# Optimization experiments

Hardware: AMD Instinct MI355X
Metric: run time of the kernel (lower is better)

Reference implementation:

```python
import jax, jax.numpy as jnp
import numpy as np

N_NODES = 50000
N_EDGES = 800000
GNN_IN, GNN_HID, GNN_OUT = 64, 128, 64
MLP_HID, MLP_OUT = 128, 1
EDGE_DIST_DIM = 16
NEG_SLOPE = 0.2


def setup_inputs() -> dict:
    key = jax.random.key(0)
    ks = jax.random.split(key, 16)
    inp = {
        "x": jax.random.normal(ks[0], (N_NODES, GNN_IN), dtype=jnp.float32),
        "edge_index": jax.random.randint(ks[1], (N_EDGES, 2), 0, N_NODES, dtype=jnp.int32),
        "edge_dist": jax.random.normal(ks[2], (N_EDGES, EDGE_DIST_DIM), dtype=jnp.float32),
        # GATConv layer 1
        "W_g1": jax.random.normal(ks[3], (GNN_IN, GNN_HID), dtype=jnp.float32) / np.sqrt(GNN_IN),
        "a1_src": jax.random.normal(ks[4], (GNN_HID,), dtype=jnp.float32) / np.sqrt(GNN_HID),
        "a1_dst": jax.random.normal(ks[5], (GNN_HID,), dtype=jnp.float32) / np.sqrt(GNN_HID),
        "b_g1": jnp.zeros((GNN_HID,), dtype=jnp.float32),
        # GATConv layer 2
        "W_g2": jax.random.normal(ks[6], (GNN_HID, GNN_OUT), dtype=jnp.float32) / np.sqrt(GNN_HID),
        "a2_src": jax.random.normal(ks[7], (GNN_OUT,), dtype=jnp.float32) / np.sqrt(GNN_OUT),
        "a2_dst": jax.random.normal(ks[8], (GNN_OUT,), dtype=jnp.float32) / np.sqrt(GNN_OUT),
        "b_g2": jnp.zeros((GNN_OUT,), dtype=jnp.float32),
        # edge MLP: in = (GNN_IN + GNN_OUT)*2 + EDGE_DIST_DIM = 272
        "W_m1": jax.random.normal(ks[9], ((GNN_IN + GNN_OUT) * 2 + EDGE_DIST_DIM, MLP_HID), dtype=jnp.float32) / np.sqrt((GNN_IN + GNN_OUT) * 2 + EDGE_DIST_DIM),
        "b_m1": jnp.zeros((MLP_HID,), dtype=jnp.float32),
        "W_m2": jax.random.normal(ks[10], (MLP_HID, MLP_OUT), dtype=jnp.float32) / np.sqrt(MLP_HID),
        "b_m2": jnp.zeros((MLP_OUT,), dtype=jnp.float32),
    }
    return inp


def gat_conv(x, src, dst, W, a_src, a_dst, bias, n_nodes):
    """Single-head GATConv (PyG defaults: self-loops already included in src/dst)."""
    h = x @ W                                # (N, out)
    alpha_s = h @ a_src                      # (N,)
    alpha_d = h @ a_dst                      # (N,)
    e = jax.nn.leaky_relu(alpha_s[src] + alpha_d[dst], NEG_SLOPE)  # (E,)
    # segment softmax over incoming edges of each destination node
    e_max = jax.ops.segment_max(e, dst, num_segments=n_nodes)
    w = jnp.exp(e - e_max[dst])
    denom = jax.ops.segment_sum(w, dst, num_segments=n_nodes)
    alpha = w / (denom[dst] + 1e-16)
    out = jax.ops.segment_sum(alpha[:, None] * h[src], dst, num_segments=n_nodes)
    return out + bias


def reference(x, edge_index, edge_dist,
              W_g1, a1_src, a1_dst, b_g1,
              W_g2, a2_src, a2_dst, b_g2,
              W_m1, b_m1, W_m2, b_m2):
    n = x.shape[0]
    row = edge_index[:, 0]
    col = edge_index[:, 1]
    # undirected edges + self loops (PyG GATConv add_self_loops=True)
    loops = jnp.arange(n, dtype=edge_index.dtype)
    src = jnp.concatenate([row, col, loops])
    dst = jnp.concatenate([col, row, loops])

    f = jax.nn.relu(gat_conv(x, src, dst, W_g1, a1_src, a1_dst, b_g1, n))
    f = jax.nn.relu(gat_conv(f, src, dst, W_g2, a2_src, a2_dst, b_g2, n))

    xf = jnp.concatenate([x, f], axis=1)     # (N, gnn_in+gnn_out)
    edge_attr = jnp.concatenate([xf[row], xf[col], edge_dist], axis=1)  # (E, 272)
    h = jax.nn.relu(edge_attr @ W_m1 + b_m1)
    return jax.nn.sigmoid(h @ W_m2 + b_m2)   # (E, 1)
```

## Files before the change

kernel.cpp:

```cpp
#include <hip/hip_runtime.h>
#include <hip/hip_bf16.h>
#include <math.h>


#define GIN 64
#define GHID 128
#define GOUT 64

typedef unsigned int u32;
typedef unsigned short u16;

__device__ __forceinline__ float bflo(u32 u) {
  union { u32 i; float f; } c; c.i = u << 16; return c.f;
}
__device__ __forceinline__ float bfhi(u32 u) {
  union { u32 i; float f; } c; c.i = u & 0xffff0000u; return c.f;
}
__device__ __forceinline__ u16 f2bf(float x) {
  __hip_bfloat16 h = __float2bfloat16(x);
  return *reinterpret_cast<u16*>(&h);
}


__global__ void hist_kernel(const int* __restrict__ eidx, int* __restrict__ deg,
                            int nE, int n) {
  int tot = 2 * nE + n;
  for (int i = blockIdx.x * blockDim.x + threadIdx.x; i < tot;
       i += gridDim.x * blockDim.x) {
    int dst;
    if (i < nE) dst = eidx[2 * i + 1];
    else if (i < 2 * nE) dst = eidx[2 * (i - nE)];
    else dst = i - 2 * nE;
    atomicAdd(&deg[dst], 1);
  }
}

#define SCAN_CHUNK 1024
__global__ void scan_partial(const int* __restrict__ deg, int* __restrict__ bsum,
                             int n) {
  int b = blockIdx.x, tid = threadIdx.x;
  int base = b * SCAN_CHUNK + tid * 4;
  int s = 0;
#pragma unroll
  for (int c = 0; c < 4; ++c) { int i = base + c; if (i < n) s += deg[i]; }
#pragma unroll
  for (int off = 32; off; off >>= 1) s += __shfl_xor(s, off, 64);
  __shared__ int ws[4];
  if ((tid & 63) == 0) ws[tid >> 6] = s;
  __syncthreads();
  if (tid == 0) bsum[b] = ws[0] + ws[1] + ws[2] + ws[3];
}
__global__ void scan_bsums(const int* __restrict__ bsum, int* __restrict__ bscan,
                           int* __restrict__ offs, int nb, int n) {
  int lane = threadIdx.x;
  int v = (lane < nb) ? bsum[lane] : 0;
  int incl = v;
#pragma unroll
  for (int off = 1; off < 64; off <<= 1) {
    int t = __shfl_up(incl, off, 64);
    if (lane >= off) incl += t;
  }
  if (lane < nb) bscan[lane] = incl - v;
  if (lane == 63) offs[n] = incl;
}
__global__ void scan_final(const int* __restrict__ deg, const int* __restrict__ bscan,
                           int* __restrict__ offs, int* __restrict__ cursor, int n) {
  int b = blockIdx.x, tid = threadIdx.x;
  int base = b * SCAN_CHUNK + tid * 4;
  int v[4]; int s = 0;
#pragma unroll
  for (int c = 0; c < 4; ++c) { int i = base + c; v[c] = (i < n) ? deg[i] : 0; s += v[c]; }
  int lane = tid & 63, wv = tid >> 6;
  int incl = s;
#pragma unroll
  for (int off = 1; off < 64; off <<= 1) {
    int t = __shfl_up(incl, off, 64);
    if (lane >= off) incl += t;
  }
  __shared__ int ws[4];
  if (lane == 63) ws[wv] = incl;
  __syncthreads();
  int woff = 0;
  for (int w2 = 0; w2 < wv; ++w2) woff += ws[w2];
  int excl = bscan[b] + woff + incl - s;
#pragma unroll
  for (int c = 0; c < 4; ++c) {
    int i = base + c;
    if (i < n) { offs[i] = excl; cursor[i] = excl; }
    excl += v[c];
  }
}

__global__ void scatter_kernel(const int* __restrict__ eidx, int* __restrict__ cursor,
                               int* __restrict__ csr, int nE, int n) {
  int tot = 2 * nE + n;
  for (int i = blockIdx.x * blockDim.x + threadIdx.x; i < tot;
       i += gridDim.x * blockDim.x) {
    int src, dst;
    if (i < nE)          { src = eidx[2 * i];            dst = eidx[2 * i + 1]; }
    else if (i < 2 * nE) { src = eidx[2 * (i - nE) + 1]; dst = eidx[2 * (i - nE)]; }
    else                 { src = i - 2 * nE;             dst = src; }
    int pos = atomicAdd(&cursor[dst], 1);
    csr[pos] = src;
  }
}


template <bool SCORES>
__global__ __launch_bounds__(256) void gemm_bf(
    const float* __restrict__ A, const float* __restrict__ A2, int ksp,
    int lda, int lda2,
    const float* __restrict__ B, int bskip, int ldb,
    u16* __restrict__ Cb, int ldcb,
    const float* __restrict__ av, const float* __restrict__ bv,
    float* __restrict__ as_, float* __restrict__ ad_,
    int M, int K) {
  __shared__ float As[32][68];
  __shared__ float Bs[32][64];
  int tid = threadIdx.x;
  int m0 = blockIdx.x * 64;
  int n0 = blockIdx.y * 64;
  const float* Bp = B + (size_t)(n0 >> 7) * bskip;
  int nb0 = n0 & 127;
  int tx = tid & 15, ty = tid >> 4;
  float acc[4][4] = {};
  for (int k0 = 0; k0 < K; k0 += 32) {
    const float* Asrc; int Alda; int kk;
    if (k0 < ksp) { Asrc = A;  Alda = lda;  kk = k0; }
    else          { Asrc = A2; Alda = lda2; kk = k0 - ksp; }
#pragma unroll
    for (int r = 0; r < 2; ++r) {
      int m = (tid >> 3) + r * 32;
      int k = (tid & 7) * 4;
      float4 v = make_float4(0.f, 0.f, 0.f, 0.f);
      int gm = m0 + m;
      if (gm < M) v = *reinterpret_cast<const float4*>(&Asrc[(size_t)gm * Alda + kk + k]);
      As[k + 0][m] = v.x; As[k + 1][m] = v.y; As[k + 2][m] = v.z; As[k + 3][m] = v.w;
    }
#pragma unroll
    for (int r = 0; r < 2; ++r) {
      int k = (tid >> 4) + r * 16;
      int nn = (tid & 15) * 4;
      float4 v = *reinterpret_cast<const float4*>(&Bp[(size_t)(k0 + k) * ldb + nb0 + nn]);
      *reinterpret_cast<float4*>(&Bs[k][nn]) = v;
    }
    __syncthreads();
#pragma unroll
    for (int k = 0; k < 32; ++k) {
      float a[4], b[4];
#pragma unroll
      for (int i = 0; i < 4; ++i) a[i] = As[k][ty * 4 + i];
#pragma unroll
      for (int i = 0; i < 4; ++i) b[i] = Bs[k][tx * 4 + i];
#pragma unroll
      for (int i = 0; i < 4; ++i)
#pragma unroll
        for (int j = 0; j < 4; ++j) acc[i][j] += a[i] * b[j];
    }
    __syncthreads();
  }
  float avv[4], bvv[4];
  if constexpr (SCORES) {
#pragma unroll
    for (int j = 0; j < 4; ++j) {
      avv[j] = av[n0 + tx * 4 + j];
      bvv[j] = bv[n0 + tx * 4 + j];
    }
  }
#pragma unroll
  for (int i = 0; i < 4; ++i) {
    int gm = m0 + ty * 4 + i;
    bool inb = gm < M;
    if (inb) {
      u16* bp = &Cb[(size_t)gm * ldcb + n0 + tx * 4];
      *reinterpret_cast<ushort4*>(bp) = make_ushort4(
          f2bf(acc[i][0]), f2bf(acc[i][1]), f2bf(acc[i][2]), f2bf(acc[i][3]));
    }
    if constexpr (SCORES) {
      float ps = acc[i][0] * avv[0] + acc[i][1] * avv[1] +
                 acc[i][2] * avv[2] + acc[i][3] * avv[3];
      float pd = acc[i][0] * bvv[0] + acc[i][1] * bvv[1] +
                 acc[i][2] * bvv[2] + acc[i][3] * bvv[3];
#pragma unroll
      for (int off = 1; off < 16; off <<= 1) {
        ps += __shfl_xor(ps, off, 16);
        pd += __shfl_xor(pd, off, 16);
      }
      if (tx == 0 && inb) {
        atomicAdd(&as_[gm], ps);
        atomicAdd(&ad_[gm], pd);
      }
    }
  }
}


__global__ __launch_bounds__(256) void gat_agg1(
    const u16* __restrict__ hb, const float* __restrict__ as_,
    const float* __restrict__ ad_, const int* __restrict__ offs,
    const int* __restrict__ csr, const float* __restrict__ bias,
    float* __restrict__ out, int n) {
  int node = blockIdx.x * 4 + (threadIdx.x >> 6);
  if (node >= n) return;
  int lane = threadIdx.x & 63;
  int g = lane >> 5, sl = lane & 31;
  int beg = offs[node], end = offs[node + 1];
  float adn = ad_[node];
  float m = -1e30f;
  for (int i = beg + lane; i < end; i += 64) {
    float v = as_[csr[i]] + adn;
    v = (v > 0.f) ? v : 0.2f * v;
    m = fmaxf(m, v);
  }
#pragma unroll
  for (int off = 32; off; off >>= 1) m = fmaxf(m, __shfl_xor(m, off, 64));
  float denom = 0.f;
  float a[4] = {0.f, 0.f, 0.f, 0.f};
  int i = beg + g;
  int s = (i < end) ? csr[i] : -1;
  uint2 pv = make_uint2(0, 0); float e = 0.f;
  if (s >= 0) {
    pv = *reinterpret_cast<const uint2*>(&hb[(size_t)s * 128 + sl * 4]);
    e = as_[s] + adn;
  }
  while (s >= 0) {
    int i2 = i + 2;
    int s2 = (i2 < end) ? csr[i2] : -1;
    uint2 pv2 = make_uint2(0, 0); float e2 = 0.f;
    if (s2 >= 0) {
      pv2 = *reinterpret_cast<const uint2*>(&hb[(size_t)s2 * 128 + sl * 4]);
      e2 = as_[s2] + adn;
    }
    e = (e > 0.f) ? e : 0.2f * e;
    float wgt = __expf(e - m);
    denom += wgt;
    a[0] += wgt * bflo(pv.x); a[1] += wgt * bfhi(pv.x);
    a[2] += wgt * bflo(pv.y); a[3] += wgt * bfhi(pv.y);
    i = i2; s = s2; pv = pv2; e = e2;
  }
  denom += __shfl_xor(denom, 32, 64);
#pragma unroll
  for (int j = 0; j < 4; ++j) a[j] += __shfl_xor(a[j], 32, 64);
  if (g == 0) {
    float inv = 1.f / (denom + 1e-16f);
    float4 bv4 = *reinterpret_cast<const float4*>(&bias[sl * 4]);
    float4 o;
    o.x = fmaxf(a[0] * inv + bv4.x, 0.f);
    o.y = fmaxf(a[1] * inv + bv4.y, 0.f);
    o.z = fmaxf(a[2] * inv + bv4.z, 0.f);
    o.w = fmaxf(a[3] * inv + bv4.w, 0.f);
    *reinterpret_cast<float4*>(&out[(size_t)node * 128 + sl * 4]) = o;
  }
}


__global__ __launch_bounds__(256) void gat_agg2(
    const u16* __restrict__ hb, const float* __restrict__ as_,
    const float* __restrict__ ad_, const int* __restrict__ offs,
    const int* __restrict__ csr, const float* __restrict__ bias,
    float* __restrict__ out, int n) {
  int node = blockIdx.x * 4 + (threadIdx.x >> 6);
  if (node >= n) return;
  int lane = threadIdx.x & 63;
  int g = lane >> 4, sl = lane & 15;
  int beg = offs[node], end = offs[node + 1];
  float adn = ad_[node];
  float m = -1e30f;
  for (int i = beg + lane; i < end; i += 64) {
    float v = as_[csr[i]] + adn;
    v = (v > 0.f) ? v : 0.2f * v;
    m = fmaxf(m, v);
  }
#pragma unroll
  for (int off = 32; off; off >>= 1) m = fmaxf(m, __shfl_xor(m, off, 64));
  float denom = 0.f;
  float a[4] = {0.f, 0.f, 0.f, 0.f};
  int i = beg + g;
  int s = (i < end) ? csr[i] : -1;
  uint2 pv = make_uint2(0, 0); float e = 0.f;
  if (s >= 0) {
    pv = *reinterpret_cast<const uint2*>(&hb[(size_t)s * 64 + sl * 4]);
    e = as_[s] + adn;
  }
  while (s >= 0) {
    int i2 = i + 4;
    int s2 = (i2 < end) ? csr[i2] : -1;
    uint2 pv2 = make_uint2(0, 0); float e2 = 0.f;
    if (s2 >= 0) {
      pv2 = *reinterpret_cast<const uint2*>(&hb[(size_t)s2 * 64 + sl * 4]);
      e2 = as_[s2] + adn;
    }
    e = (e > 0.f) ? e : 0.2f * e;
    float wgt = __expf(e - m);
    denom += wgt;
    a[0] += wgt * bflo(pv.x); a[1] += wgt * bfhi(pv.x);
    a[2] += wgt * bflo(pv.y); a[3] += wgt * bfhi(pv.y);
    i = i2; s = s2; pv = pv2; e = e2;
  }
  denom += __shfl_xor(denom, 16, 64);
  denom += __shfl_xor(denom, 32, 64);
#pragma unroll
  for (int j = 0; j < 4; ++j) {
    a[j] += __shfl_xor(a[j], 16, 64);
    a[j] += __shfl_xor(a[j], 32, 64);
  }
  if (lane < 16) {
    float inv = 1.f / (denom + 1e-16f);
    float4 bv4 = *reinterpret_cast<const float4*>(&bias[sl * 4]);
    float4 o;
    o.x = fmaxf(a[0] * inv + bv4.x, 0.f);
    o.y = fmaxf(a[1] * inv + bv4.y, 0.f);
    o.z = fmaxf(a[2] * inv + bv4.z, 0.f);
    o.w = fmaxf(a[3] * inv + bv4.w, 0.f);
    *reinterpret_cast<float4*>(&out[(size_t)node * 64 + sl * 4]) = o;
  }
}


__global__ __launch_bounds__(256) void edge_mlp(
    const int* __restrict__ eidx, const float* __restrict__ dist,
    const u16* __restrict__ Pb, const float* __restrict__ W3,
    const float* __restrict__ b1, const float* __restrict__ W2,
    const float* __restrict__ b2, float* __restrict__ out, int nE) {
  __shared__ float4 W3s[16][32];
  int tid = threadIdx.x;
  for (int idx = tid; idx < 16 * 32; idx += 256) {
    int k = idx >> 5, q = idx & 31;
    W3s[k][q] = *reinterpret_cast<const float4*>(&W3[k * 128 + q * 4]);
  }
  __syncthreads();
  int lane = tid & 63, wv = tid >> 6;
  int g = lane >> 4, sl = lane & 15;
  float4 b1a = *reinterpret_cast<const float4*>(&b1[sl * 8]);
  float4 b1b = *reinterpret_cast<const float4*>(&b1[sl * 8 + 4]);
  float4 w2a = *reinterpret_cast<const float4*>(&W2[sl * 8]);
  float4 w2b = *reinterpret_cast<const float4*>(&W2[sl * 8 + 4]);
  float b2v = b2[0];
  for (int e0 = (blockIdx.x * 4 + wv) * 4; e0 < nE; e0 += gridDim.x * 16) {
    int e = e0 + g;
    bool valid = e < nE;
    int ee = valid ? e : 0;
    int r = eidx[2 * ee], c = eidx[2 * ee + 1];
    uint4 p1 = *reinterpret_cast<const uint4*>(&Pb[(size_t)r * 256 + sl * 8]);
    uint4 p2 = *reinterpret_cast<const uint4*>(&Pb[(size_t)c * 256 + 128 + sl * 8]);
    float dsl = dist[(size_t)ee * 16 + sl];
    float a[8];
    a[0] = bflo(p1.x) + bflo(p2.x) + b1a.x;
    a[1] = bfhi(p1.x) + bfhi(p2.x) + b1a.y;
    a[2] = bflo(p1.y) + bflo(p2.y) + b1a.z;
    a[3] = bfhi(p1.y) + bfhi(p2.y) + b1a.w;
    a[4] = bflo(p1.z) + bflo(p2.z) + b1b.x;
    a[5] = bfhi(p1.z) + bfhi(p2.z) + b1b.y;
    a[6] = bflo(p1.w) + bflo(p2.w) + b1b.z;
    a[7] = bfhi(p1.w) + bfhi(p2.w) + b1b.w;
#pragma unroll
    for (int k = 0; k < 16; ++k) {
      float dk = __shfl(dsl, (g << 4) + k, 64);
      float4 wA = W3s[k][2 * sl];
      float4 wB = W3s[k][2 * sl + 1];
      a[0] += dk * wA.x; a[1] += dk * wA.y; a[2] += dk * wA.z; a[3] += dk * wA.w;
      a[4] += dk * wB.x; a[5] += dk * wB.y; a[6] += dk * wB.z; a[7] += dk * wB.w;
    }
    float p = fmaxf(a[0], 0.f) * w2a.x + fmaxf(a[1], 0.f) * w2a.y +
              fmaxf(a[2], 0.f) * w2a.z + fmaxf(a[3], 0.f) * w2a.w +
              fmaxf(a[4], 0.f) * w2b.x + fmaxf(a[5], 0.f) * w2b.y +
              fmaxf(a[6], 0.f) * w2b.z + fmaxf(a[7], 0.f) * w2b.w;
#pragma unroll
    for (int off = 1; off < 16; off <<= 1) p += __shfl_xor(p, off, 16);
    if (valid && sl == 0) out[e] = 1.f / (1.f + __expf(-(p + b2v)));
  }
}


extern "C" void kernel_launch(void* const* d_in, const int* in_sizes, int n_in,
                              void* d_out, int out_size, void* d_ws, size_t ws_size,
                              hipStream_t stream) {
  const float* x      = (const float*)d_in[0];
  const int*   eidx   = (const int*)d_in[1];
  const float* dist   = (const float*)d_in[2];
  const float* W_g1   = (const float*)d_in[3];
  const float* a1_src = (const float*)d_in[4];
  const float* a1_dst = (const float*)d_in[5];
  const float* b_g1   = (const float*)d_in[6];
  const float* W_g2   = (const float*)d_in[7];
  const float* a2_src = (const float*)d_in[8];
  const float* a2_dst = (const float*)d_in[9];
  const float* b_g2   = (const float*)d_in[10];
  const float* W_m1   = (const float*)d_in[11];
  const float* b_m1   = (const float*)d_in[12];
  const float* W_m2   = (const float*)d_in[13];
  const float* b_m2   = (const float*)d_in[14];
  float* out = (float*)d_out;

  const int n  = in_sizes[0] / GIN;
  const int nE = in_sizes[1] / 2;
  const int ndir = 2 * nE + n;

  char* w = (char*)d_ws;
  size_t off = 0;
  auto alloc = [&](size_t bytes) {
    size_t o = off;
    off += (bytes + 255) & ~(size_t)255;
    return o;
  };
  size_t o_deg    = alloc((size_t)n * 4);
  size_t o_offs   = alloc((size_t)(n + 1) * 4);
  size_t o_cursor = alloc((size_t)n * 4);
  size_t o_as1    = alloc((size_t)n * 4);
  size_t o_ad1    = alloc((size_t)n * 4);
  size_t o_as2    = alloc((size_t)n * 4);
  size_t o_ad2    = alloc((size_t)n * 4);
  size_t o_bsum   = alloc(64 * 4);
  size_t o_bscan  = alloc(64 * 4);
  size_t o_csr    = alloc((size_t)ndir * 4);
  size_t o_big    = alloc((size_t)n * 256 * 2);
  size_t o_f1     = alloc((size_t)n * GHID * 4);
  size_t o_f2     = alloc((size_t)n * GOUT * 4);
  (void)ws_size;

  int*   deg    = (int*)(w + o_deg);
  int*   offs   = (int*)(w + o_offs);
  int*   cursor = (int*)(w + o_cursor);
  float* as1    = (float*)(w + o_as1);
  float* ad1    = (float*)(w + o_ad1);
  float* as2    = (float*)(w + o_as2);
  float* ad2    = (float*)(w + o_ad2);
  int*   bsum   = (int*)(w + o_bsum);
  int*   bscan  = (int*)(w + o_bscan);
  int*   csr    = (int*)(w + o_csr);
  u16*   h1b    = (u16*)(w + o_big);
  u16*   h2b    = (u16*)(w + o_big + (size_t)n * GHID * 2);
  u16*   Pb     = (u16*)(w + o_big);
  float* f1     = (float*)(w + o_f1);
  float* f2     = (float*)(w + o_f2);

  hipMemsetAsync(deg, 0, (size_t)n * 4, stream);
  hipMemsetAsync(as1, 0, (size_t)n * 4, stream);
  hipMemsetAsync(ad1, 0, (size_t)n * 4, stream);
  hipMemsetAsync(as2, 0, (size_t)n * 4, stream);
  hipMemsetAsync(ad2, 0, (size_t)n * 4, stream);
  hist_kernel<<<2048, 256, 0, stream>>>(eidx, deg, nE, n);
  int nb = (n + SCAN_CHUNK - 1) / SCAN_CHUNK;
  scan_partial<<<nb, 256, 0, stream>>>(deg, bsum, n);
  scan_bsums<<<1, 64, 0, stream>>>(bsum, bscan, offs, nb, n);
  scan_final<<<nb, 256, 0, stream>>>(deg, bscan, offs, cursor, n);
  scatter_kernel<<<2048, 256, 0, stream>>>(eidx, cursor, csr, nE, n);

  const int mtiles = (n + 63) / 64;
  const int BIGK = 1 << 30;

  gemm_bf<true><<<dim3(mtiles, 2), 256, 0, stream>>>(
      x, x, BIGK, GIN, GIN, W_g1, 0, GHID, h1b, GHID,
      a1_src, a1_dst, as1, ad1, n, GIN);

  gat_agg1<<<(n + 3) / 4, 256, 0, stream>>>(h1b, as1, ad1, offs, csr, b_g1, f1, n);

  gemm_bf<true><<<dim3(mtiles, 1), 256, 0, stream>>>(
      f1, f1, BIGK, GHID, GHID, W_g2, 0, GOUT, h2b, GOUT,
      a2_src, a2_dst, as2, ad2, n, GHID);

  gat_agg2<<<(n + 3) / 4, 256, 0, stream>>>(h2b, as2, ad2, offs, csr, b_g2, f2, n);

  gemm_bf<false><<<dim3(mtiles, 4), 256, 0, stream>>>(
      x, f2, GIN, GIN, GOUT, W_m1, 128 * 128, GHID, Pb, 256,
      nullptr, nullptr, nullptr, nullptr, n, GHID);

  edge_mlp<<<4096, 256, 0, stream>>>(eidx, dist, Pb, W_m1 + 256 * 128, b_m1, W_m2, b_m2,
                                     out, nE);
}
```

Measured before the change: 719.1 us.

## Sort edges by source for MLP locality, widen GAT gathers, drop softmax max pass

Adds a counting sort of the original edges by source row (a histogram, scan and scatter into ra/ce arrays), so the edge MLP visits edges grouped by source node and reuses the Pb row loads. The GAT aggregation kernels now load 16-byte bf16 vectors per lane and process more edges per wave in parallel. They also drop the max-subtraction pass of the segment softmax, which risks exp overflow for large logits. The sort adds several kernels and extra workspace, and the edge_mlp reads of dist and writes of out become scattered.

```diff
diff --git a/kernel.cpp b/kernel.cpp
--- a/kernel.cpp
+++ b/kernel.cpp
@@ -32,6 +32,14 @@
     else if (i < 2 * nE) dst = eidx[2 * (i - nE)];
     else dst = i - 2 * nE;
     atomicAdd(&deg[dst], 1);
+  }
+}
+
+__global__ void hist_r(const int* __restrict__ eidx, int* __restrict__ deg2,
+                       int nE) {
+  for (int e = blockIdx.x * blockDim.x + threadIdx.x; e < nE;
+       e += gridDim.x * blockDim.x) {
+    atomicAdd(&deg2[eidx[2 * e]], 1);
   }
 }
 
@@ -102,6 +110,17 @@
     else                 { src = i - 2 * nE;             dst = src; }
     int pos = atomicAdd(&cursor[dst], 1);
     csr[pos] = src;
+  }
+}
+
+__global__ void scatter_r(const int* __restrict__ eidx, int* __restrict__ cur2,
+                          int* __restrict__ ra, int2* __restrict__ ce, int nE) {
+  for (int e = blockIdx.x * blockDim.x + threadIdx.x; e < nE;
+       e += gridDim.x * blockDim.x) {
+    int r = eidx[2 * e], c = eidx[2 * e + 1];
+    int pos = atomicAdd(&cur2[r], 1);
+    ra[pos] = r;
+    ce[pos] = make_int2(c, e);
   }
 }
 
@@ -203,53 +222,57 @@
   int node = blockIdx.x * 4 + (threadIdx.x >> 6);
   if (node >= n) return;
   int lane = threadIdx.x & 63;
-  int g = lane >> 5, sl = lane & 31;
+  int g = lane >> 4, sl = lane & 15;
   int beg = offs[node], end = offs[node + 1];
   float adn = ad_[node];
-  float m = -1e30f;
-  for (int i = beg + lane; i < end; i += 64) {
-    float v = as_[csr[i]] + adn;
-    v = (v > 0.f) ? v : 0.2f * v;
-    m = fmaxf(m, v);
-  }
-#pragma unroll
-  for (int off = 32; off; off >>= 1) m = fmaxf(m, __shfl_xor(m, off, 64));
   float denom = 0.f;
-  float a[4] = {0.f, 0.f, 0.f, 0.f};
+  float a[8] = {};
   int i = beg + g;
   int s = (i < end) ? csr[i] : -1;
-  uint2 pv = make_uint2(0, 0); float e = 0.f;
+  uint4 pv = make_uint4(0, 0, 0, 0); float e = 0.f;
   if (s >= 0) {
-    pv = *reinterpret_cast<const uint2*>(&hb[(size_t)s * 128 + sl * 4]);
+    pv = *reinterpret_cast<const uint4*>(&hb[(size_t)s * 128 + sl * 8]);
     e = as_[s] + adn;
   }
   while (s >= 0) {
-    int i2 = i + 2;
+    int i2 = i + 4;
     int s2 = (i2 < end) ? csr[i2] : -1;
-    uint2 pv2 = make_uint2(0, 0); float e2 = 0.f;
+    uint4 pv2 = make_uint4(0, 0, 0, 0); float e2 = 0.f;
     if (s2 >= 0) {
-      pv2 = *reinterpret_cast<const uint2*>(&hb[(size_t)s2 * 128 + sl * 4]);
+      pv2 = *reinterpret_cast<const uint4*>(&hb[(size_t)s2 * 128 + sl * 8]);
       e2 = as_[s2] + adn;
     }
     e = (e > 0.f) ? e : 0.2f * e;
-    float wgt = __expf(e - m);
+    float wgt = __expf(e);
     denom += wgt;
     a[0] += wgt * bflo(pv.x); a[1] += wgt * bfhi(pv.x);
     a[2] += wgt * bflo(pv.y); a[3] += wgt * bfhi(pv.y);
+    a[4] += wgt * bflo(pv.z); a[5] += wgt * bfhi(pv.z);
+    a[6] += wgt * bflo(pv.w); a[7] += wgt * bfhi(pv.w);
     i = i2; s = s2; pv = pv2; e = e2;
   }
+  denom += __shfl_xor(denom, 16, 64);
   denom += __shfl_xor(denom, 32, 64);
 #pragma unroll
-  for (int j = 0; j < 4; ++j) a[j] += __shfl_xor(a[j], 32, 64);
+  for (int j = 0; j < 8; ++j) {
+    a[j] += __shfl_xor(a[j], 16, 64);
+    a[j] += __shfl_xor(a[j], 32, 64);
+  }
   if (g == 0) {
     float inv = 1.f / (denom + 1e-16f);
-    float4 bv4 = *reinterpret_cast<const float4*>(&bias[sl * 4]);
-    float4 o;
-    o.x = fmaxf(a[0] * inv + bv4.x, 0.f);
-    o.y = fmaxf(a[1] * inv + bv4.y, 0.f);
-    o.z = fmaxf(a[2] * inv + bv4.z, 0.f);
-    o.w = fmaxf(a[3] * inv + bv4.w, 0.f);
-    *reinterpret_cast<float4*>(&out[(size_t)node * 128 + sl * 4]) = o;
+    float4 b0 = *reinterpret_cast<const float4*>(&bias[sl * 8]);
+    float4 b1v = *reinterpret_cast<const float4*>(&bias[sl * 8 + 4]);
+    float4 o0, o1;
+    o0.x = fmaxf(a[0] * inv + b0.x, 0.f);
+    o0.y = fmaxf(a[1] * inv + b0.y, 0.f);
+    o0.z = fmaxf(a[2] * inv + b0.z, 0.f);
+    o0.w = fmaxf(a[3] * inv + b0.w, 0.f);
+    o1.x = fmaxf(a[4] * inv + b1v.x, 0.f);
+    o1.y = fmaxf(a[5] * inv + b1v.y, 0.f);
+    o1.z = fmaxf(a[6] * inv + b1v.z, 0.f);
+    o1.w = fmaxf(a[7] * inv + b1v.w, 0.f);
+    *reinterpret_cast<float4*>(&out[(size_t)node * 128 + sl * 8]) = o0;
+    *reinterpret_cast<float4*>(&out[(size_t)node * 128 + sl * 8 + 4]) = o1;
   }
 }
 
@@ -262,63 +285,66 @@
   int node = blockIdx.x * 4 + (threadIdx.x >> 6);
   if (node >= n) return;
   int lane = threadIdx.x & 63;
-  int g = lane >> 4, sl = lane & 15;
+  int g = lane >> 3, sl = lane & 7;
   int beg = offs[node], end = offs[node + 1];
   float adn = ad_[node];
-  float m = -1e30f;
-  for (int i = beg + lane; i < end; i += 64) {
-    float v = as_[csr[i]] + adn;
-    v = (v > 0.f) ? v : 0.2f * v;
-    m = fmaxf(m, v);
-  }
-#pragma unroll
-  for (int off = 32; off; off >>= 1) m = fmaxf(m, __shfl_xor(m, off, 64));
   float denom = 0.f;
-  float a[4] = {0.f, 0.f, 0.f, 0.f};
+  float a[8] = {};
   int i = beg + g;
   int s = (i < end) ? csr[i] : -1;
-  uint2 pv = make_uint2(0, 0); float e = 0.f;
+  uint4 pv = make_uint4(0, 0, 0, 0); float e = 0.f;
   if (s >= 0) {
-    pv = *reinterpret_cast<const uint2*>(&hb[(size_t)s * 64 + sl * 4]);
+    pv = *reinterpret_cast<const uint4*>(&hb[(size_t)s * 64 + sl * 8]);
     e = as_[s] + adn;
   }
   while (s >= 0) {
-    int i2 = i + 4;
+    int i2 = i + 8;
     int s2 = (i2 < end) ? csr[i2] : -1;
-    uint2 pv2 = make_uint2(0, 0); float e2 = 0.f;
+    uint4 pv2 = make_uint4(0, 0, 0, 0); float e2 = 0.f;
     if (s2 >= 0) {
-      pv2 = *reinterpret_cast<const uint2*>(&hb[(size_t)s2 * 64 + sl * 4]);
+      pv2 = *reinterpret_cast<const uint4*>(&hb[(size_t)s2 * 64 + sl * 8]);
       e2 = as_[s2] + adn;
     }
     e = (e > 0.f) ? e : 0.2f * e;
-    float wgt = __expf(e - m);
+    float wgt = __expf(e);
     denom += wgt;
     a[0] += wgt * bflo(pv.x); a[1] += wgt * bfhi(pv.x);
     a[2] += wgt * bflo(pv.y); a[3] += wgt * bfhi(pv.y);
+    a[4] += wgt * bflo(pv.z); a[5] += wgt * bfhi(pv.z);
+    a[6] += wgt * bflo(pv.w); a[7] += wgt * bfhi(pv.w);
     i = i2; s = s2; pv = pv2; e = e2;
   }
+  denom += __shfl_xor(denom, 8, 64);
   denom += __shfl_xor(denom, 16, 64);
   denom += __shfl_xor(denom, 32, 64);
 #pragma unroll
-  for (int j = 0; j < 4; ++j) {
+  for (int j = 0; j < 8; ++j) {
+    a[j] += __shfl_xor(a[j], 8, 64);
     a[j] += __shfl_xor(a[j], 16, 64);
     a[j] += __shfl_xor(a[j], 32, 64);
   }
-  if (lane < 16) {
+  if (g == 0) {
     float inv = 1.f / (denom + 1e-16f);
-    float4 bv4 = *reinterpret_cast<const float4*>(&bias[sl * 4]);
-    float4 o;
-    o.x = fmaxf(a[0] * inv + bv4.x, 0.f);
-    o.y = fmaxf(a[1] * inv + bv4.y, 0.f);
-    o.z = fmaxf(a[2] * inv + bv4.z, 0.f);
-    o.w = fmaxf(a[3] * inv + bv4.w, 0.f);
-    *reinterpret_cast<float4*>(&out[(size_t)node * 64 + sl * 4]) = o;
+    float4 b0 = *reinterpret_cast<const float4*>(&bias[sl * 8]);
+    float4 b1v = *reinterpret_cast<const float4*>(&bias[sl * 8 + 4]);
+    float4 o0, o1;
+    o0.x = fmaxf(a[0] * inv + b0.x, 0.f);
+    o0.y = fmaxf(a[1] * inv + b0.y, 0.f);
+    o0.z = fmaxf(a[2] * inv + b0.z, 0.f);
+    o0.w = fmaxf(a[3] * inv + b0.w, 0.f);
+    o1.x = fmaxf(a[4] * inv + b1v.x, 0.f);
+    o1.y = fmaxf(a[5] * inv + b1v.y, 0.f);
+    o1.z = fmaxf(a[6] * inv + b1v.z, 0.f);
+    o1.w = fmaxf(a[7] * inv + b1v.w, 0.f);
+    *reinterpret_cast<float4*>(&out[(size_t)node * 64 + sl * 8]) = o0;
+    *reinterpret_cast<float4*>(&out[(size_t)node * 64 + sl * 8 + 4]) = o1;
   }
 }
 
 
 __global__ __launch_bounds__(256) void edge_mlp(
-    const int* __restrict__ eidx, const float* __restrict__ dist,
+    const int* __restrict__ ra, const int2* __restrict__ ce,
+    const float* __restrict__ dist,
     const u16* __restrict__ Pb, const float* __restrict__ W3,
     const float* __restrict__ b1, const float* __restrict__ W2,
     const float* __restrict__ b2, float* __restrict__ out, int nE) {
@@ -336,14 +362,16 @@
   float4 w2a = *reinterpret_cast<const float4*>(&W2[sl * 8]);
   float4 w2b = *reinterpret_cast<const float4*>(&W2[sl * 8 + 4]);
   float b2v = b2[0];
-  for (int e0 = (blockIdx.x * 4 + wv) * 4; e0 < nE; e0 += gridDim.x * 16) {
-    int e = e0 + g;
-    bool valid = e < nE;
-    int ee = valid ? e : 0;
-    int r = eidx[2 * ee], c = eidx[2 * ee + 1];
+  for (int p0 = (blockIdx.x * 4 + wv) * 4; p0 < nE; p0 += gridDim.x * 16) {
+    int p = p0 + g;
+    bool valid = p < nE;
+    int pp = valid ? p : 0;
+    int r = ra[pp];
+    int2 cece = ce[pp];
+    int c = cece.x, e = cece.y;
     uint4 p1 = *reinterpret_cast<const uint4*>(&Pb[(size_t)r * 256 + sl * 8]);
     uint4 p2 = *reinterpret_cast<const uint4*>(&Pb[(size_t)c * 256 + 128 + sl * 8]);
-    float dsl = dist[(size_t)ee * 16 + sl];
+    float dsl = dist[(size_t)e * 16 + sl];
     float a[8];
     a[0] = bflo(p1.x) + bflo(p2.x) + b1a.x;
     a[1] = bfhi(p1.x) + bfhi(p2.x) + b1a.y;
@@ -361,13 +389,13 @@
       a[0] += dk * wA.x; a[1] += dk * wA.y; a[2] += dk * wA.z; a[3] += dk * wA.w;
       a[4] += dk * wB.x; a[5] += dk * wB.y; a[6] += dk * wB.z; a[7] += dk * wB.w;
     }
-    float p = fmaxf(a[0], 0.f) * w2a.x + fmaxf(a[1], 0.f) * w2a.y +
-              fmaxf(a[2], 0.f) * w2a.z + fmaxf(a[3], 0.f) * w2a.w +
-              fmaxf(a[4], 0.f) * w2b.x + fmaxf(a[5], 0.f) * w2b.y +
-              fmaxf(a[6], 0.f) * w2b.z + fmaxf(a[7], 0.f) * w2b.w;
-#pragma unroll
-    for (int off = 1; off < 16; off <<= 1) p += __shfl_xor(p, off, 16);
-    if (valid && sl == 0) out[e] = 1.f / (1.f + __expf(-(p + b2v)));
+    float p_ = fmaxf(a[0], 0.f) * w2a.x + fmaxf(a[1], 0.f) * w2a.y +
+               fmaxf(a[2], 0.f) * w2a.z + fmaxf(a[3], 0.f) * w2a.w +
+               fmaxf(a[4], 0.f) * w2b.x + fmaxf(a[5], 0.f) * w2b.y +
+               fmaxf(a[6], 0.f) * w2b.z + fmaxf(a[7], 0.f) * w2b.w;
+#pragma unroll
+    for (int off = 1; off < 16; off <<= 1) p_ += __shfl_xor(p_, off, 16);
+    if (valid && sl == 0) out[e] = 1.f / (1.f + __expf(-(p_ + b2v)));
   }
 }
 
@@ -406,6 +434,8 @@
   size_t o_deg    = alloc((size_t)n * 4);
   size_t o_offs   = alloc((size_t)(n + 1) * 4);
   size_t o_cursor = alloc((size_t)n * 4);
+  size_t o_deg2   = alloc((size_t)n * 4);
+  size_t o_offs2  = alloc((size_t)(n + 1) * 4);
   size_t o_as1    = alloc((size_t)n * 4);
   size_t o_ad1    = alloc((size_t)n * 4);
   size_t o_as2    = alloc((size_t)n * 4);
@@ -413,6 +443,8 @@
   size_t o_bsum   = alloc(64 * 4);
   size_t o_bscan  = alloc(64 * 4);
   size_t o_csr    = alloc((size_t)ndir * 4);
+  size_t o_ra     = alloc((size_t)nE * 4);
+  size_t o_ce     = alloc((size_t)nE * 8);
   size_t o_big    = alloc((size_t)n * 256 * 2);
   size_t o_f1     = alloc((size_t)n * GHID * 4);
   size_t o_f2     = alloc((size_t)n * GOUT * 4);
@@ -421,6 +453,8 @@
   int*   deg    = (int*)(w + o_deg);
   int*   offs   = (int*)(w + o_offs);
   int*   cursor = (int*)(w + o_cursor);
+  int*   deg2   = (int*)(w + o_deg2);
+  int*   cur2   = (int*)(w + o_offs2);
   float* as1    = (float*)(w + o_as1);
   float* ad1    = (float*)(w + o_ad1);
   float* as2    = (float*)(w + o_as2);
@@ -428,6 +462,8 @@
   int*   bsum   = (int*)(w + o_bsum);
   int*   bscan  = (int*)(w + o_bscan);
   int*   csr    = (int*)(w + o_csr);
+  int*   ra     = (int*)(w + o_ra);
+  int2*  ce     = (int2*)(w + o_ce);
   u16*   h1b    = (u16*)(w + o_big);
   u16*   h2b    = (u16*)(w + o_big + (size_t)n * GHID * 2);
   u16*   Pb     = (u16*)(w + o_big);
@@ -435,16 +471,22 @@
   float* f2     = (float*)(w + o_f2);
 
   hipMemsetAsync(deg, 0, (size_t)n * 4, stream);
+  hipMemsetAsync(deg2, 0, (size_t)n * 4, stream);
   hipMemsetAsync(as1, 0, (size_t)n * 4, stream);
   hipMemsetAsync(ad1, 0, (size_t)n * 4, stream);
   hipMemsetAsync(as2, 0, (size_t)n * 4, stream);
   hipMemsetAsync(ad2, 0, (size_t)n * 4, stream);
   hist_kernel<<<2048, 256, 0, stream>>>(eidx, deg, nE, n);
+  hist_r<<<1024, 256, 0, stream>>>(eidx, deg2, nE);
   int nb = (n + SCAN_CHUNK - 1) / SCAN_CHUNK;
   scan_partial<<<nb, 256, 0, stream>>>(deg, bsum, n);
   scan_bsums<<<1, 64, 0, stream>>>(bsum, bscan, offs, nb, n);
   scan_final<<<nb, 256, 0, stream>>>(deg, bscan, offs, cursor, n);
   scatter_kernel<<<2048, 256, 0, stream>>>(eidx, cursor, csr, nE, n);
+  scan_partial<<<nb, 256, 0, stream>>>(deg2, bsum, n);
+  scan_bsums<<<1, 64, 0, stream>>>(bsum, bscan, (int*)(w + o_offs2), nb, n);
+  scan_final<<<nb, 256, 0, stream>>>(deg2, bscan, deg2 , cur2, n);
+  scatter_r<<<1024, 256, 0, stream>>>(eidx, cur2, ra, ce, nE);
 
   const int mtiles = (n + 63) / 64;
   const int BIGK = 1 << 30;
@@ -465,6 +507,6 @@
       x, f2, GIN, GIN, GOUT, W_m1, 128 * 128, GHID, Pb, 256,
       nullptr, nullptr, nullptr, nullptr, n, GHID);
 
-  edge_mlp<<<4096, 256, 0, stream>>>(eidx, dist, Pb, W_m1 + 256 * 128, b_m1, W_m2, b_m2,
-                                     out, nE);
-}
+  edge_mlp<<<4096, 256, 0, stream>>>(ra, ce, dist, Pb, W_m1 + 256 * 128, b_m1,
+                                     W_m2, b_m2, out, nE);
+}
```

Result: slower. 781.3 us (+8.7%).

## Drop softmax max pass, widen GAT gathers, and software-pipeline edge MLP loads

Applied to the files above, without the earlier changes.

Both GAT aggregation kernels no longer run the separate pass that computes the per-node max logit. They now exponentiate the raw leaky-relu scores directly, which saves a second gather over csr and as_ but can overflow if logits grow large. Each lane now loads 16 bf16 features, so more edges are processed in parallel per wave, at the cost of wider cross-lane reductions. The edge MLP reads edge indices as int2 and prefetches the next edge's rows and dist values one iteration ahead to hide gather latency, which raises register use.

```diff
diff --git a/kernel.cpp b/kernel.cpp
--- a/kernel.cpp
+++ b/kernel.cpp
@@ -203,53 +203,69 @@
   int node = blockIdx.x * 4 + (threadIdx.x >> 6);
   if (node >= n) return;
   int lane = threadIdx.x & 63;
-  int g = lane >> 5, sl = lane & 31;
+  int g = lane >> 3, sl = lane & 7;
   int beg = offs[node], end = offs[node + 1];
   float adn = ad_[node];
-  float m = -1e30f;
-  for (int i = beg + lane; i < end; i += 64) {
-    float v = as_[csr[i]] + adn;
-    v = (v > 0.f) ? v : 0.2f * v;
-    m = fmaxf(m, v);
-  }
-#pragma unroll
-  for (int off = 32; off; off >>= 1) m = fmaxf(m, __shfl_xor(m, off, 64));
   float denom = 0.f;
-  float a[4] = {0.f, 0.f, 0.f, 0.f};
-  int i = beg + g;
-  int s = (i < end) ? csr[i] : -1;
-  uint2 pv = make_uint2(0, 0); float e = 0.f;
-  if (s >= 0) {
-    pv = *reinterpret_cast<const uint2*>(&hb[(size_t)s * 128 + sl * 4]);
-    e = as_[s] + adn;
-  }
-  while (s >= 0) {
-    int i2 = i + 2;
+  float a[16] = {};
+  int i0 = beg + g;
+  int s0 = (i0 < end) ? csr[i0] : -1;
+  uint4 pa0 = make_uint4(0,0,0,0), pb0 = make_uint4(0,0,0,0); float e0 = 0.f;
+  if (s0 >= 0) {
+    const u16* row = &hb[(size_t)s0 * 128 + sl * 16];
+    pa0 = *reinterpret_cast<const uint4*>(row);
+    pb0 = *reinterpret_cast<const uint4*>(row + 8);
+    e0 = as_[s0] + adn;
+  }
+  int i1 = i0 + 8;
+  int s1 = (i1 < end) ? csr[i1] : -1;
+  while (s0 >= 0) {
+    int i2 = i1 + 8;
     int s2 = (i2 < end) ? csr[i2] : -1;
-    uint2 pv2 = make_uint2(0, 0); float e2 = 0.f;
-    if (s2 >= 0) {
-      pv2 = *reinterpret_cast<const uint2*>(&hb[(size_t)s2 * 128 + sl * 4]);
-      e2 = as_[s2] + adn;
-    }
-    e = (e > 0.f) ? e : 0.2f * e;
-    float wgt = __expf(e - m);
+    uint4 pa1 = make_uint4(0,0,0,0), pb1 = make_uint4(0,0,0,0); float e1 = 0.f;
+    if (s1 >= 0) {
+      const u16* row = &hb[(size_t)s1 * 128 + sl * 16];
+      pa1 = *reinterpret_cast<const uint4*>(row);
+      pb1 = *reinterpret_cast<const uint4*>(row + 8);
+      e1 = as_[s1] + adn;
+    }
+    float e = (e0 > 0.f) ? e0 : 0.2f * e0;
+    float wgt = __expf(e);
     denom += wgt;
-    a[0] += wgt * bflo(pv.x); a[1] += wgt * bfhi(pv.x);
-    a[2] += wgt * bflo(pv.y); a[3] += wgt * bfhi(pv.y);
-    i = i2; s = s2; pv = pv2; e = e2;
-  }
+    a[0]  += wgt * bflo(pa0.x); a[1]  += wgt * bfhi(pa0.x);
+    a[2]  += wgt * bflo(pa0.y); a[3]  += wgt * bfhi(pa0.y);
+    a[4]  += wgt * bflo(pa0.z); a[5]  += wgt * bfhi(pa0.z);
+    a[6]  += wgt * bflo(pa0.w); a[7]  += wgt * bfhi(pa0.w);
+    a[8]  += wgt * bflo(pb0.x); a[9]  += wgt * bfhi(pb0.x);
+    a[10] += wgt * bflo(pb0.y); a[11] += wgt * bfhi(pb0.y);
+    a[12] += wgt * bflo(pb0.z); a[13] += wgt * bfhi(pb0.z);
+    a[14] += wgt * bflo(pb0.w); a[15] += wgt * bfhi(pb0.w);
+    s0 = s1; pa0 = pa1; pb0 = pb1; e0 = e1;
+    s1 = s2; i1 = i2;
+  }
+  denom += __shfl_xor(denom, 8, 64);
+  denom += __shfl_xor(denom, 16, 64);
   denom += __shfl_xor(denom, 32, 64);
 #pragma unroll
-  for (int j = 0; j < 4; ++j) a[j] += __shfl_xor(a[j], 32, 64);
+  for (int j = 0; j < 16; ++j) {
+    a[j] += __shfl_xor(a[j], 8, 64);
+    a[j] += __shfl_xor(a[j], 16, 64);
+    a[j] += __shfl_xor(a[j], 32, 64);
+  }
   if (g == 0) {
     float inv = 1.f / (denom + 1e-16f);
-    float4 bv4 = *reinterpret_cast<const float4*>(&bias[sl * 4]);
-    float4 o;
-    o.x = fmaxf(a[0] * inv + bv4.x, 0.f);
-    o.y = fmaxf(a[1] * inv + bv4.y, 0.f);
-    o.z = fmaxf(a[2] * inv + bv4.z, 0.f);
-    o.w = fmaxf(a[3] * inv + bv4.w, 0.f);
-    *reinterpret_cast<float4*>(&out[(size_t)node * 128 + sl * 4]) = o;
+    float* op = &out[(size_t)node * 128 + sl * 16];
+    const float* bp = &bias[sl * 16];
+#pragma unroll
+    for (int q = 0; q < 4; ++q) {
+      float4 bq = *reinterpret_cast<const float4*>(bp + q * 4);
+      float4 o;
+      o.x = fmaxf(a[q * 4 + 0] * inv + bq.x, 0.f);
+      o.y = fmaxf(a[q * 4 + 1] * inv + bq.y, 0.f);
+      o.z = fmaxf(a[q * 4 + 2] * inv + bq.z, 0.f);
+      o.w = fmaxf(a[q * 4 + 3] * inv + bq.w, 0.f);
+      *reinterpret_cast<float4*>(op + q * 4) = o;
+    }
   }
 }
 
@@ -262,63 +278,75 @@
   int node = blockIdx.x * 4 + (threadIdx.x >> 6);
   if (node >= n) return;
   int lane = threadIdx.x & 63;
-  int g = lane >> 4, sl = lane & 15;
+  int g = lane >> 2, sl = lane & 3;
   int beg = offs[node], end = offs[node + 1];
   float adn = ad_[node];
-  float m = -1e30f;
-  for (int i = beg + lane; i < end; i += 64) {
-    float v = as_[csr[i]] + adn;
-    v = (v > 0.f) ? v : 0.2f * v;
-    m = fmaxf(m, v);
-  }
-#pragma unroll
-  for (int off = 32; off; off >>= 1) m = fmaxf(m, __shfl_xor(m, off, 64));
   float denom = 0.f;
-  float a[4] = {0.f, 0.f, 0.f, 0.f};
-  int i = beg + g;
-  int s = (i < end) ? csr[i] : -1;
-  uint2 pv = make_uint2(0, 0); float e = 0.f;
-  if (s >= 0) {
-    pv = *reinterpret_cast<const uint2*>(&hb[(size_t)s * 64 + sl * 4]);
-    e = as_[s] + adn;
-  }
-  while (s >= 0) {
-    int i2 = i + 4;
+  float a[16] = {};
+  int i0 = beg + g;
+  int s0 = (i0 < end) ? csr[i0] : -1;
+  uint4 pa0 = make_uint4(0,0,0,0), pb0 = make_uint4(0,0,0,0); float e0 = 0.f;
+  if (s0 >= 0) {
+    const u16* row = &hb[(size_t)s0 * 64 + sl * 16];
+    pa0 = *reinterpret_cast<const uint4*>(row);
+    pb0 = *reinterpret_cast<const uint4*>(row + 8);
+    e0 = as_[s0] + adn;
+  }
+  int i1 = i0 + 16;
+  int s1 = (i1 < end) ? csr[i1] : -1;
+  while (s0 >= 0) {
+    int i2 = i1 + 16;
     int s2 = (i2 < end) ? csr[i2] : -1;
-    uint2 pv2 = make_uint2(0, 0); float e2 = 0.f;
-    if (s2 >= 0) {
-      pv2 = *reinterpret_cast<const uint2*>(&hb[(size_t)s2 * 64 + sl * 4]);
-      e2 = as_[s2] + adn;
-    }
-    e = (e > 0.f) ? e : 0.2f * e;
-    float wgt = __expf(e - m);
+    uint4 pa1 = make_uint4(0,0,0,0), pb1 = make_uint4(0,0,0,0); float e1 = 0.f;
+    if (s1 >= 0) {
+      const u16* row = &hb[(size_t)s1 * 64 + sl * 16];
+      pa1 = *reinterpret_cast<const uint4*>(row);
+      pb1 = *reinterpret_cast<const uint4*>(row + 8);
+      e1 = as_[s1] + adn;
+    }
+    float e = (e0 > 0.f) ? e0 : 0.2f * e0;
+    float wgt = __expf(e);
     denom += wgt;
-    a[0] += wgt * bflo(pv.x); a[1] += wgt * bfhi(pv.x);
-    a[2] += wgt * bflo(pv.y); a[3] += wgt * bfhi(pv.y);
-    i = i2; s = s2; pv = pv2; e = e2;
-  }
-  denom += __shfl_xor(denom, 16, 64);
-  denom += __shfl_xor(denom, 32, 64);
-#pragma unroll
-  for (int j = 0; j < 4; ++j) {
+    a[0]  += wgt * bflo(pa0.x); a[1]  += wgt * bfhi(pa0.x);
+    a[2]  += wgt * bflo(pa0.y); a[3]  += wgt * bfhi(pa0.y);
+    a[4]  += wgt * bflo(pa0.z); a[5]  += wgt * bfhi(pa0.z);
+    a[6]  += wgt * bflo(pa0.w); a[7]  += wgt * bfhi(pa0.w);
+    a[8]  += wgt * bflo(pb0.x); a[9]  += wgt * bfhi(pb0.x);
+    a[10] += wgt * bflo(pb0.y); a[11] += wgt * bfhi(pb0.y);
+    a[12] += wgt * bflo(pb0.z); a[13] += wgt * bfhi(pb0.z);
+    a[14] += wgt * bflo(pb0.w); a[15] += wgt * bfhi(pb0.w);
+    s0 = s1; pa0 = pa1; pb0 = pb1; e0 = e1;
+    s1 = s2; i1 = i2;
+  }
+#pragma unroll
+  for (int w2 = 4; w2 < 64; w2 <<= 1) denom += __shfl_xor(denom, w2, 64);
+#pragma unroll
+  for (int j = 0; j < 16; ++j) {
+    a[j] += __shfl_xor(a[j], 4, 64);
+    a[j] += __shfl_xor(a[j], 8, 64);
     a[j] += __shfl_xor(a[j], 16, 64);
     a[j] += __shfl_xor(a[j], 32, 64);
   }
-  if (lane < 16) {
+  if (g == 0) {
     float inv = 1.f / (denom + 1e-16f);
-    float4 bv4 = *reinterpret_cast<const float4*>(&bias[sl * 4]);
-    float4 o;
-    o.x = fmaxf(a[0] * inv + bv4.x, 0.f);
-    o.y = fmaxf(a[1] * inv + bv4.y, 0.f);
-    o.z = fmaxf(a[2] * inv + bv4.z, 0.f);
-    o.w = fmaxf(a[3] * inv + bv4.w, 0.f);
-    *reinterpret_cast<float4*>(&out[(size_t)node * 64 + sl * 4]) = o;
+    float* op = &out[(size_t)node * 64 + sl * 16];
+    const float* bp = &bias[sl * 16];
+#pragma unroll
+    for (int q = 0; q < 4; ++q) {
+      float4 bq = *reinterpret_cast<const float4*>(bp + q * 4);
+      float4 o;
+      o.x = fmaxf(a[q * 4 + 0] * inv + bq.x, 0.f);
+      o.y = fmaxf(a[q * 4 + 1] * inv + bq.y, 0.f);
+      o.z = fmaxf(a[q * 4 + 2] * inv + bq.z, 0.f);
+      o.w = fmaxf(a[q * 4 + 3] * inv + bq.w, 0.f);
+      *reinterpret_cast<float4*>(op + q * 4) = o;
+    }
   }
 }
 
 
 __global__ __launch_bounds__(256) void edge_mlp(
-    const int* __restrict__ eidx, const float* __restrict__ dist,
+    const int2* __restrict__ eidx, const float* __restrict__ dist,
     const u16* __restrict__ Pb, const float* __restrict__ W3,
     const float* __restrict__ b1, const float* __restrict__ W2,
     const float* __restrict__ b2, float* __restrict__ out, int nE) {
@@ -336,14 +364,29 @@
   float4 w2a = *reinterpret_cast<const float4*>(&W2[sl * 8]);
   float4 w2b = *reinterpret_cast<const float4*>(&W2[sl * 8 + 4]);
   float b2v = b2[0];
-  for (int e0 = (blockIdx.x * 4 + wv) * 4; e0 < nE; e0 += gridDim.x * 16) {
-    int e = e0 + g;
-    bool valid = e < nE;
-    int ee = valid ? e : 0;
-    int r = eidx[2 * ee], c = eidx[2 * ee + 1];
-    uint4 p1 = *reinterpret_cast<const uint4*>(&Pb[(size_t)r * 256 + sl * 8]);
-    uint4 p2 = *reinterpret_cast<const uint4*>(&Pb[(size_t)c * 256 + 128 + sl * 8]);
-    float dsl = dist[(size_t)ee * 16 + sl];
+  const int stride = gridDim.x * 16;
+  int e0 = (blockIdx.x * 4 + wv) * 4 + g;
+  bool v0 = e0 < nE;
+  int2 rc0 = v0 ? eidx[e0] : make_int2(0, 0);
+  uint4 p1 = make_uint4(0,0,0,0), p2 = make_uint4(0,0,0,0); float ds0 = 0.f;
+  if (v0) {
+    p1 = *reinterpret_cast<const uint4*>(&Pb[(size_t)rc0.x * 256 + sl * 8]);
+    p2 = *reinterpret_cast<const uint4*>(&Pb[(size_t)rc0.y * 256 + 128 + sl * 8]);
+    ds0 = dist[(size_t)e0 * 16 + sl];
+  }
+  int e1 = e0 + stride;
+  bool v1 = e1 < nE;
+  int2 rc1 = v1 ? eidx[e1] : make_int2(0, 0);
+  while (v0) {
+    int e2 = e1 + stride;
+    bool v2 = e2 < nE;
+    int2 rc2 = v2 ? eidx[e2] : make_int2(0, 0);
+    uint4 q1 = make_uint4(0,0,0,0), q2 = make_uint4(0,0,0,0); float ds1 = 0.f;
+    if (v1) {
+      q1 = *reinterpret_cast<const uint4*>(&Pb[(size_t)rc1.x * 256 + sl * 8]);
+      q2 = *reinterpret_cast<const uint4*>(&Pb[(size_t)rc1.y * 256 + 128 + sl * 8]);
+      ds1 = dist[(size_t)e1 * 16 + sl];
+    }
     float a[8];
     a[0] = bflo(p1.x) + bflo(p2.x) + b1a.x;
     a[1] = bfhi(p1.x) + bfhi(p2.x) + b1a.y;
@@ -355,19 +398,21 @@
     a[7] = bfhi(p1.w) + bfhi(p2.w) + b1b.w;
 #pragma unroll
     for (int k = 0; k < 16; ++k) {
-      float dk = __shfl(dsl, (g << 4) + k, 64);
+      float dk = __shfl(ds0, (g << 4) + k, 64);
       float4 wA = W3s[k][2 * sl];
       float4 wB = W3s[k][2 * sl + 1];
       a[0] += dk * wA.x; a[1] += dk * wA.y; a[2] += dk * wA.z; a[3] += dk * wA.w;
       a[4] += dk * wB.x; a[5] += dk * wB.y; a[6] += dk * wB.z; a[7] += dk * wB.w;
     }
-    float p = fmaxf(a[0], 0.f) * w2a.x + fmaxf(a[1], 0.f) * w2a.y +
-              fmaxf(a[2], 0.f) * w2a.z + fmaxf(a[3], 0.f) * w2a.w +
-              fmaxf(a[4], 0.f) * w2b.x + fmaxf(a[5], 0.f) * w2b.y +
-              fmaxf(a[6], 0.f) * w2b.z + fmaxf(a[7], 0.f) * w2b.w;
-#pragma unroll
-    for (int off = 1; off < 16; off <<= 1) p += __shfl_xor(p, off, 16);
-    if (valid && sl == 0) out[e] = 1.f / (1.f + __expf(-(p + b2v)));
+    float p_ = fmaxf(a[0], 0.f) * w2a.x + fmaxf(a[1], 0.f) * w2a.y +
+               fmaxf(a[2], 0.f) * w2a.z + fmaxf(a[3], 0.f) * w2a.w +
+               fmaxf(a[4], 0.f) * w2b.x + fmaxf(a[5], 0.f) * w2b.y +
+               fmaxf(a[6], 0.f) * w2b.z + fmaxf(a[7], 0.f) * w2b.w;
+#pragma unroll
+    for (int off = 1; off < 16; off <<= 1) p_ += __shfl_xor(p_, off, 16);
+    if (sl == 0) out[e0] = 1.f / (1.f + __expf(-(p_ + b2v)));
+    e0 = e1; v0 = v1; p1 = q1; p2 = q2; ds0 = ds1;
+    e1 = e2; v1 = v2; rc1 = rc2;
   }
 }
 
@@ -465,6 +510,6 @@
       x, f2, GIN, GIN, GOUT, W_m1, 128 * 128, GHID, Pb, 256,
       nullptr, nullptr, nullptr, nullptr, n, GHID);
 
-  edge_mlp<<<4096, 256, 0, stream>>>(eidx, dist, Pb, W_m1 + 256 * 128, b_m1, W_m2, b_m2,
-                                     out, nE);
-}
+  edge_mlp<<<4096, 256, 0, stream>>>((const int2*)eidx, dist, Pb,
+                                     W_m1 + 256 * 128, b_m1, W_m2, b_m2, out, nE);
+}
```

After: 651.5 us. 1.1x faster.
